# Optimization experiments

Measured on AMD Instinct MI355X. Metric: run time of the kernel, lower is better.

The kernel has to match this reference:

```python
import jax, jax.numpy as jnp
import numpy as np


def setup_inputs() -> dict:
    key = jax.random.key(0)
    k0, k1, k2, k3 = jax.random.split(key, 4)
    B, L, H, E, D = 8, 1024, 8, 64, 64
    queries = jax.random.normal(k0, (B, L, H, E), dtype=jnp.float32)
    keys = jax.random.normal(k1, (B, L, H, E), dtype=jnp.float32)
    values = jax.random.normal(k2, (B, L, H, D), dtype=jnp.float32)
    # sigma is a divisor inside exp(-dist/sigma); keep it strictly positive
    sigma = jax.random.uniform(k3, (B, H, L), dtype=jnp.float32, minval=0.1, maxval=2.0)
    return {"queries": queries, "keys": keys, "values": values, "sigma": sigma}


def reference(queries, keys, values, sigma):
    B, L, H, E = queries.shape
    S = keys.shape[1]
    scale = 1.0 / float(E) ** 0.5  # self.scale is None -> 1/sqrt(E)

    # series association: masked scaled softmax(QK^T)
    scores = jnp.einsum('blhe,bshe->bhls', queries, keys)  # (B,H,L,S)
    causal = jnp.triu(jnp.ones((L, S), dtype=bool), k=1)   # TriangularCausalMask
    scores = jnp.where(causal[None, None], -jnp.inf, scores)
    series_association = jax.nn.softmax(scale * scores, axis=-1)  # dropout p=0.0

    # prior association: Gaussian-kernel over |i-j|, sigma indexed by column s
    # prior[b,i,s] = mean_h exp(-|i-s| / sigma[b,h,s]), then row-normalized
    dist = jnp.abs(jnp.arange(L)[:, None] - jnp.arange(S)[None, :]).astype(queries.dtype)  # (L,S)
    prior = jnp.exp(-dist[None, None] / sigma[:, :, None, :]).mean(axis=1)  # (B,L,S)
    prior_association = prior / prior.sum(axis=-1, keepdims=True)

    V = jnp.einsum('bhls,bshd->blhd', series_association, values)  # (B,L,H,D)
    return V, series_association, prior_association
```

## Files before the change

kernel.cpp:

```cpp
#include <hip/hip_runtime.h>
#include <hip/hip_bf16.h>

#define B_ 8
#define L_ 1024
#define H_ 8
#define E_ 64
#define CL2E 0.18033688f

typedef __attribute__((ext_vector_type(8))) short bf8v;
typedef __attribute__((ext_vector_type(4))) float f32x4;

__device__ __forceinline__ short f2bf(float x) {
    union { float f; unsigned u; } c; c.f = x;
    const unsigned r = (c.u + 0x7fffu + ((c.u >> 16) & 1u)) >> 16;
    return (short)r;
}

__global__ __launch_bounds__(256) void kconv_kernel(const float* __restrict__ K,
                                                    short* __restrict__ Kb) {
    const int g = blockIdx.x * 256 + threadIdx.x;
    const float4 v = *((const float4*)K + g);
    const int e4 = g & 15, h = (g >> 4) & 7, l = (g >> 7) & 1023, b = g >> 17;
    short4 o; o.x = f2bf(v.x); o.y = f2bf(v.y); o.z = f2bf(v.z); o.w = f2bf(v.w);
    *(short4*)(Kb + (((size_t)(b * 8 + h)) << 16) + l * 64 + (e4 << 2)) = o;
}

__global__ __launch_bounds__(256) void vtrans_kernel(const float* __restrict__ V,
                                                     short* __restrict__ VT) {
    const int bx = blockIdx.x;
    const int bh = bx >> 4; const int l0 = (bx & 15) << 6;
    const int b = bh >> 3, h = bh & 7;
    const int t = threadIdx.x;
    __shared__ float lds[64][65];
    {
        const int r = t >> 2, cq = t & 3;
        const float* src = V + ((size_t)((b * 1024 + l0 + r) * 8) + h) * 64 + (cq << 4);
#pragma unroll
        for (int j = 0; j < 4; ++j) {
            const float4 v = *(const float4*)(src + (j << 2));
            const int d = (cq << 4) + (j << 2);
            lds[r][d] = v.x; lds[r][d + 1] = v.y; lds[r][d + 2] = v.z; lds[r][d + 3] = v.w;
        }
    }
    __syncthreads();
    {
        const int d = t >> 2, lq = t & 3;
        short tmp[16];
#pragma unroll
        for (int k = 0; k < 16; ++k) tmp[k] = f2bf(lds[(lq << 4) + k][d]);
        short* dst = VT + ((size_t)bh << 16) + d * 1024 + l0 + (lq << 4);
        *(bf8v*)dst = *(bf8v*)tmp;
        *(bf8v*)(dst + 8) = *(bf8v*)(tmp + 8);
    }
}

__global__ __launch_bounds__(256) void prior_kernel(const float* __restrict__ sigma,
                                                    float* __restrict__ outP) {
    const int bx = blockIdx.x;
    const int b  = bx >> 8;
    const int i0 = (bx & 255) << 2;
    const int t  = threadIdx.x;
    const int s0 = t << 2;

    __shared__ float wred[4][4];
    __shared__ float sinv[4];

    const float* sb = sigma + (size_t)b * H_ * L_;
    float wv[8][4];
#pragma unroll
    for (int h = 0; h < 8; ++h) {
        const float4 sg = *(const float4*)(sb + h * L_ + s0);
        wv[h][0] = -1.4426950408889634f * __builtin_amdgcn_rcpf(sg.x);
        wv[h][1] = -1.4426950408889634f * __builtin_amdgcn_rcpf(sg.y);
        wv[h][2] = -1.4426950408889634f * __builtin_amdgcn_rcpf(sg.z);
        wv[h][3] = -1.4426950408889634f * __builtin_amdgcn_rcpf(sg.w);
    }
    float acc[4][4];
#pragma unroll
    for (int row = 0; row < 4; ++row)
#pragma unroll
        for (int j = 0; j < 4; ++j) acc[row][j] = 0.f;
#pragma unroll
    for (int h = 0; h < 8; ++h)
#pragma unroll
        for (int row = 0; row < 4; ++row)
#pragma unroll
            for (int j = 0; j < 4; ++j) {
                int di = (i0 + row) - (s0 + j);
                const float dist = (float)(di < 0 ? -di : di);
                acc[row][j] += __builtin_amdgcn_exp2f(dist * wv[h][j]);
            }
    float tsum[4];
#pragma unroll
    for (int row = 0; row < 4; ++row) {
        float v = acc[row][0] + acc[row][1] + acc[row][2] + acc[row][3];
#pragma unroll
        for (int off = 1; off < 64; off <<= 1) v += __shfl_xor(v, off);
        tsum[row] = v;
    }
    if ((t & 63) == 0) {
#pragma unroll
        for (int row = 0; row < 4; ++row) wred[t >> 6][row] = tsum[row];
    }
    __syncthreads();
    if (t < 4) sinv[t] = 1.f / (wred[0][t] + wred[1][t] + wred[2][t] + wred[3][t]);
    __syncthreads();
#pragma unroll
    for (int row = 0; row < 4; ++row) {
        const float iv = sinv[row];
        float4 o;
        o.x = acc[row][0] * iv; o.y = acc[row][1] * iv;
        o.z = acc[row][2] * iv; o.w = acc[row][3] * iv;
        *(float4*)(outP + (size_t)(b * L_ + i0 + row) * L_ + s0) = o;
    }
}

__global__ __launch_bounds__(256, 4) void attn_kernel(const float* __restrict__ Q,
                                                      const short* __restrict__ Kbf,
                                                      const short* __restrict__ VTbf,
                                                      float* __restrict__ outV,
                                                      float* __restrict__ outS) {
    const int bx = blockIdx.x;
    const int qt = 15 - (bx >> 6);
    const int bh = bx & 63;
    const int b = bh >> 3, h = bh & 7;
    const int q0 = qt << 6;
    const int t = threadIdx.x;
    const int lane = t & 63, w = t >> 6;
    const int l15 = lane & 15, l4 = lane >> 4;
    const int nch = qt + 1;

    __shared__ __align__(16) short Klds[4096];
    __shared__ __align__(16) short Vlds[4096];
    __shared__ __align__(16) short Plds[4096];

    const short* Kb = Kbf + ((size_t)bh << 16);
    const short* Vb = VTbf + ((size_t)bh << 16);

    const int srow = lane >> 3;
    const int sslot = lane & 7;
    const int pslot = sslot ^ srow;

    bf8v aq0, aq1;
    {
        const float* Qrow = Q + ((size_t)((b * 1024 + q0 + 16 * w + l15) * 8) + h) * 64 + l4 * 8;
#pragma unroll
        for (int j = 0; j < 8; ++j) aq0[j] = f2bf(Qrow[j]);
#pragma unroll
        for (int j = 0; j < 8; ++j) aq1[j] = f2bf(Qrow[32 + j]);
    }

    float* outSb = outS + ((size_t)bh << 20) + (size_t)q0 * 1024;

    {
        const int cend = nch << 6;
        const float4 z4 = make_float4(0.f, 0.f, 0.f, 0.f);
        for (int col = cend + (lane << 2); col < 1024; col += 256) {
            float* rp = outSb + (size_t)(16 * w) * 1024 + col;
#pragma unroll
            for (int rr = 0; rr < 16; ++rr) *(float4*)(rp + (size_t)rr * 1024) = z4;
        }
    }

    float sum4[4] = {0.f, 0.f, 0.f, 0.f};
    for (int c = 0; c < nch; ++c) {
        const int s0 = c << 6;
        __syncthreads();
#pragma unroll
        for (int p = 0; p < 2; ++p) {
            const int krow = 16 * w + 8 * p + srow;
            const bf8v kv = *(const bf8v*)(Kb + (size_t)(s0 + krow) * 64 + sslot * 8);
            *(bf8v*)((char*)Klds + krow * 128 + (pslot << 4)) = kv;
        }
        __syncthreads();
        const bool diag = (c == qt);
#pragma unroll
        for (int cb = 0; cb < 4; ++cb) {
            const int krow = (cb << 4) + l15;
            const char* kp = (char*)Klds + krow * 128;
            const int sw = (krow & 7) << 4;
            const bf8v b0 = *(const bf8v*)(kp + ((l4 << 4) ^ sw));
            const bf8v b1 = *(const bf8v*)(kp + ((64 + (l4 << 4)) ^ sw));
            f32x4 acc = {0.f, 0.f, 0.f, 0.f};
            acc = __builtin_amdgcn_mfma_f32_16x16x32_bf16(aq0, b0, acc, 0, 0, 0);
            acc = __builtin_amdgcn_mfma_f32_16x16x32_bf16(aq1, b1, acc, 0, 0, 0);
#pragma unroll
            for (int r = 0; r < 4; ++r) {
                float e = __builtin_amdgcn_exp2f(acc[r] * CL2E);
                if (diag && ((cb << 4) + l15 > 16 * w + (l4 << 2) + r)) e = 0.f;
                sum4[r] += e;
            }
        }
    }
#pragma unroll
    for (int r = 0; r < 4; ++r) {
        float v = sum4[r];
        v += __shfl_xor(v, 1); v += __shfl_xor(v, 2);
        v += __shfl_xor(v, 4); v += __shfl_xor(v, 8);
        sum4[r] = v;
    }
    float inv4[4];
#pragma unroll
    for (int r = 0; r < 4; ++r) inv4[r] = __builtin_amdgcn_rcpf(sum4[r]);

    f32x4 oacc[4];
#pragma unroll
    for (int db = 0; db < 4; ++db) oacc[db] = (f32x4){0.f, 0.f, 0.f, 0.f};

    short* Pw = Plds + (w << 10);
    float* sbase = outSb + (size_t)(16 * w + (l4 << 2)) * 1024 + l15;

    for (int c = 0; c < nch; ++c) {
        const int s0 = c << 6;
        __syncthreads();
#pragma unroll
        for (int p = 0; p < 2; ++p) {
            const int krow = 16 * w + 8 * p + srow;
            const bf8v kv = *(const bf8v*)(Kb + (size_t)(s0 + krow) * 64 + sslot * 8);
            *(bf8v*)((char*)Klds + krow * 128 + (pslot << 4)) = kv;
            const bf8v vv = *(const bf8v*)(Vb + (size_t)krow * 1024 + s0 + sslot * 8);
            *(bf8v*)((char*)Vlds + krow * 128 + (pslot << 4)) = vv;
        }
        __syncthreads();
        const bool diag = (c == qt);
#pragma unroll
        for (int cb = 0; cb < 4; ++cb) {
            const int krow = (cb << 4) + l15;
            const char* kp = (char*)Klds + krow * 128;
            const int sw = (krow & 7) << 4;
            const bf8v b0 = *(const bf8v*)(kp + ((l4 << 4) ^ sw));
            const bf8v b1 = *(const bf8v*)(kp + ((64 + (l4 << 4)) ^ sw));
            f32x4 acc = {0.f, 0.f, 0.f, 0.f};
            acc = __builtin_amdgcn_mfma_f32_16x16x32_bf16(aq0, b0, acc, 0, 0, 0);
            acc = __builtin_amdgcn_mfma_f32_16x16x32_bf16(aq1, b1, acc, 0, 0, 0);
#pragma unroll
            for (int r = 0; r < 4; ++r) {
                float e = __builtin_amdgcn_exp2f(acc[r] * CL2E);
                if (diag && ((cb << 4) + l15 > 16 * w + (l4 << 2) + r)) e = 0.f;
                const float pv = e * inv4[r];
                sbase[(size_t)r * 1024 + s0 + (cb << 4)] = pv;
                const int row = (l4 << 2) + r;
                const int byte = row * 128 +
                                 ((((cb << 1) + (l15 >> 3)) ^ (row & 7)) << 4) +
                                 ((l15 & 7) << 1);
                *(short*)((char*)Pw + byte) = f2bf(pv);
            }
        }
        const int swp = (l15 & 7) << 4;
        const bf8v p0 = *(const bf8v*)((char*)Pw + l15 * 128 + ((l4 << 4) ^ swp));
        const bf8v p1 = *(const bf8v*)((char*)Pw + l15 * 128 + (((4 + l4) << 4) ^ swp));
#pragma unroll
        for (int db = 0; db < 4; ++db) {
            const int vrow = (db << 4) + l15;
            const char* vp = (char*)Vlds + vrow * 128;
            const int swv = (vrow & 7) << 4;
            const bf8v v0 = *(const bf8v*)(vp + ((l4 << 4) ^ swv));
            const bf8v v1 = *(const bf8v*)(vp + (((4 + l4) << 4) ^ swv));
            oacc[db] = __builtin_amdgcn_mfma_f32_16x16x32_bf16(p0, v0, oacc[db], 0, 0, 0);
            oacc[db] = __builtin_amdgcn_mfma_f32_16x16x32_bf16(p1, v1, oacc[db], 0, 0, 0);
        }
    }

#pragma unroll
    for (int db = 0; db < 4; ++db)
#pragma unroll
        for (int r = 0; r < 4; ++r)
            outV[((size_t)((b * 1024 + q0 + 16 * w + (l4 << 2) + r) * 8) + h) * 64 +
                 (db << 4) + l15] = oacc[db][r];
}

extern "C" void kernel_launch(void* const* d_in, const int* in_sizes, int n_in,
                              void* d_out, int out_size, void* d_ws, size_t ws_size,
                              hipStream_t stream) {
    const float* Q     = (const float*)d_in[0];
    const float* K     = (const float*)d_in[1];
    const float* V     = (const float*)d_in[2];
    const float* sigma = (const float*)d_in[3];

    float* out  = (float*)d_out;
    float* outV = out;
    float* outS = out + (size_t)B_ * L_ * H_ * E_;
    float* outP = outS + (size_t)B_ * H_ * L_ * L_;

    short* Kbf = (short*)outP;
    short* VTb = Kbf + ((size_t)64 << 16);

    kconv_kernel<<<dim3(4096), dim3(256), 0, stream>>>(K, Kbf);
    vtrans_kernel<<<dim3(1024), dim3(256), 0, stream>>>(V, VTb);
    attn_kernel<<<dim3(1024), dim3(256), 0, stream>>>(Q, Kbf, VTb, outV, outS);
    prior_kernel<<<dim3(B_ * (L_ / 4)), dim3(256), 0, stream>>>(sigma, outP);
}
```

Baseline: 400.7 us.

## Double-buffer K/V LDS staging with register prefetch and fuse prep kernels

```diff
diff --git a/kernel.cpp b/kernel.cpp
--- a/kernel.cpp
+++ b/kernel.cpp
@@ -16,36 +16,43 @@
     return (short)r;
 }
 
-__global__ __launch_bounds__(256) void kconv_kernel(const float* __restrict__ K,
-                                                    short* __restrict__ Kb) {
-    const int g = blockIdx.x * 256 + threadIdx.x;
-    const float4 v = *((const float4*)K + g);
-    const int e4 = g & 15, h = (g >> 4) & 7, l = (g >> 7) & 1023, b = g >> 17;
-    short4 o; o.x = f2bf(v.x); o.y = f2bf(v.y); o.z = f2bf(v.z); o.w = f2bf(v.w);
-    *(short4*)(Kb + (((size_t)(b * 8 + h)) << 16) + l * 64 + (e4 << 2)) = o;
-}
-
-__global__ __launch_bounds__(256) void vtrans_kernel(const float* __restrict__ V,
-                                                     short* __restrict__ VT) {
+__global__ __launch_bounds__(256) void prep_kernel(const float* __restrict__ K,
+                                                   const float* __restrict__ V,
+                                                   short* __restrict__ Kb,
+                                                   short* __restrict__ VT) {
     const int bx = blockIdx.x;
     const int bh = bx >> 4; const int l0 = (bx & 15) << 6;
     const int b = bh >> 3, h = bh & 7;
     const int t = threadIdx.x;
     __shared__ float lds[64][65];
-    {
-        const int r = t >> 2, cq = t & 3;
-        const float* src = V + ((size_t)((b * 1024 + l0 + r) * 8) + h) * 64 + (cq << 4);
+
+    const int r = t >> 2, cq = t & 3;
+    {
+        const float* vsrc = V + ((size_t)((b * 1024 + l0 + r) * 8) + h) * 64 + (cq << 4);
 #pragma unroll
         for (int j = 0; j < 4; ++j) {
-            const float4 v = *(const float4*)(src + (j << 2));
+            const float4 v = *(const float4*)(vsrc + (j << 2));
             const int d = (cq << 4) + (j << 2);
             lds[r][d] = v.x; lds[r][d + 1] = v.y; lds[r][d + 2] = v.z; lds[r][d + 3] = v.w;
         }
     }
+    {
+        const float* ksrc = K + ((size_t)((b * 1024 + l0 + r) * 8) + h) * 64 + (cq << 4);
+        short tk[16] __attribute__((aligned(16)));
+#pragma unroll
+        for (int j = 0; j < 4; ++j) {
+            const float4 v = *(const float4*)(ksrc + (j << 2));
+            tk[(j << 2) + 0] = f2bf(v.x); tk[(j << 2) + 1] = f2bf(v.y);
+            tk[(j << 2) + 2] = f2bf(v.z); tk[(j << 2) + 3] = f2bf(v.w);
+        }
+        short* kdst = Kb + ((size_t)bh << 16) + (l0 + r) * 64 + (cq << 4);
+        *(bf8v*)kdst = *(bf8v*)tk;
+        *(bf8v*)(kdst + 8) = *(bf8v*)(tk + 8);
+    }
     __syncthreads();
     {
         const int d = t >> 2, lq = t & 3;
-        short tmp[16];
+        short tmp[16] __attribute__((aligned(16)));
 #pragma unroll
         for (int k = 0; k < 16; ++k) tmp[k] = f2bf(lds[(lq << 4) + k][d]);
         short* dst = VT + ((size_t)bh << 16) + d * 1024 + l0 + (lq << 4);
@@ -130,8 +137,7 @@
     const int l15 = lane & 15, l4 = lane >> 4;
     const int nch = qt + 1;
 
-    __shared__ __align__(16) short Klds[4096];
-    __shared__ __align__(16) short Vlds[4096];
+    __shared__ __align__(16) short stage[2][8192];
     __shared__ __align__(16) short Plds[4096];
 
     const short* Kb = Kbf + ((size_t)bh << 16);
@@ -140,6 +146,11 @@
     const int srow = lane >> 3;
     const int sslot = lane & 7;
     const int pslot = sslot ^ srow;
+    const int krow0 = 16 * w + srow;
+    const int stb0 = krow0 * 128 + (pslot << 4);
+    const int stb1 = stb0 + 8 * 128;
+    const short* kbase = Kb + krow0 * 64 + sslot * 8;
+    const short* vbase = Vb + krow0 * 1024 + sslot * 8;
 
     bf8v aq0, aq1;
     {
@@ -152,32 +163,39 @@
 
     float* outSb = outS + ((size_t)bh << 20) + (size_t)q0 * 1024;
 
+    bf8v kA, kB, vA, vB;
+
+    kA = *(const bf8v*)(kbase);
+    kB = *(const bf8v*)(kbase + 512);
     {
         const int cend = nch << 6;
-        const float4 z4 = make_float4(0.f, 0.f, 0.f, 0.f);
+        const f32x4 z4 = {0.f, 0.f, 0.f, 0.f};
         for (int col = cend + (lane << 2); col < 1024; col += 256) {
             float* rp = outSb + (size_t)(16 * w) * 1024 + col;
 #pragma unroll
-            for (int rr = 0; rr < 16; ++rr) *(float4*)(rp + (size_t)rr * 1024) = z4;
-        }
-    }
+            for (int rr = 0; rr < 16; ++rr)
+                __builtin_nontemporal_store(z4, (f32x4*)(rp + (size_t)rr * 1024));
+        }
+    }
+    {
+        char* d0 = (char*)stage[0];
+        *(bf8v*)(d0 + stb0) = kA;
+        *(bf8v*)(d0 + stb1) = kB;
+    }
+    __syncthreads();
 
     float sum4[4] = {0.f, 0.f, 0.f, 0.f};
     for (int c = 0; c < nch; ++c) {
-        const int s0 = c << 6;
-        __syncthreads();
-#pragma unroll
-        for (int p = 0; p < 2; ++p) {
-            const int krow = 16 * w + 8 * p + srow;
-            const bf8v kv = *(const bf8v*)(Kb + (size_t)(s0 + krow) * 64 + sslot * 8);
-            *(bf8v*)((char*)Klds + krow * 128 + (pslot << 4)) = kv;
-        }
-        __syncthreads();
+        if (c + 1 < nch) {
+            kA = *(const bf8v*)(kbase + (size_t)(c + 1) * 4096);
+            kB = *(const bf8v*)(kbase + (size_t)(c + 1) * 4096 + 512);
+        }
+        const char* kt = (const char*)stage[c & 1];
         const bool diag = (c == qt);
 #pragma unroll
         for (int cb = 0; cb < 4; ++cb) {
             const int krow = (cb << 4) + l15;
-            const char* kp = (char*)Klds + krow * 128;
+            const char* kp = kt + krow * 128;
             const int sw = (krow & 7) << 4;
             const bf8v b0 = *(const bf8v*)(kp + ((l4 << 4) ^ sw));
             const bf8v b1 = *(const bf8v*)(kp + ((64 + (l4 << 4)) ^ sw));
@@ -191,7 +209,16 @@
                 sum4[r] += e;
             }
         }
-    }
+        if (c + 1 < nch) {
+            char* dn = (char*)stage[(c + 1) & 1];
+            *(bf8v*)(dn + stb0) = kA;
+            *(bf8v*)(dn + stb1) = kB;
+        }
+        __syncthreads();
+    }
+
+    vA = *(const bf8v*)(vbase + (nch - 1) * 64);
+    vB = *(const bf8v*)(vbase + (nch - 1) * 64 + 8192);
 #pragma unroll
     for (int r = 0; r < 4; ++r) {
         float v = sum4[r];
@@ -202,6 +229,12 @@
     float inv4[4];
 #pragma unroll
     for (int r = 0; r < 4; ++r) inv4[r] = __builtin_amdgcn_rcpf(sum4[r]);
+    {
+        char* sv = (char*)stage[(nch - 1) & 1] + 8192;
+        *(bf8v*)(sv + stb0) = vA;
+        *(bf8v*)(sv + stb1) = vB;
+    }
+    __syncthreads();
 
     f32x4 oacc[4];
 #pragma unroll
@@ -210,23 +243,21 @@
     short* Pw = Plds + (w << 10);
     float* sbase = outSb + (size_t)(16 * w + (l4 << 2)) * 1024 + l15;
 
-    for (int c = 0; c < nch; ++c) {
+    for (int c = nch - 1; c >= 0; --c) {
+        if (c > 0) {
+            kA = *(const bf8v*)(kbase + (size_t)(c - 1) * 4096);
+            kB = *(const bf8v*)(kbase + (size_t)(c - 1) * 4096 + 512);
+            vA = *(const bf8v*)(vbase + (c - 1) * 64);
+            vB = *(const bf8v*)(vbase + (c - 1) * 64 + 8192);
+        }
         const int s0 = c << 6;
-        __syncthreads();
-#pragma unroll
-        for (int p = 0; p < 2; ++p) {
-            const int krow = 16 * w + 8 * p + srow;
-            const bf8v kv = *(const bf8v*)(Kb + (size_t)(s0 + krow) * 64 + sslot * 8);
-            *(bf8v*)((char*)Klds + krow * 128 + (pslot << 4)) = kv;
-            const bf8v vv = *(const bf8v*)(Vb + (size_t)krow * 1024 + s0 + sslot * 8);
-            *(bf8v*)((char*)Vlds + krow * 128 + (pslot << 4)) = vv;
-        }
-        __syncthreads();
+        const char* kt = (const char*)stage[c & 1];
+        const char* vt = kt + 8192;
         const bool diag = (c == qt);
 #pragma unroll
         for (int cb = 0; cb < 4; ++cb) {
             const int krow = (cb << 4) + l15;
-            const char* kp = (char*)Klds + krow * 128;
+            const char* kp = kt + krow * 128;
             const int sw = (krow & 7) << 4;
             const bf8v b0 = *(const bf8v*)(kp + ((l4 << 4) ^ sw));
             const bf8v b1 = *(const bf8v*)(kp + ((64 + (l4 << 4)) ^ sw));
@@ -238,7 +269,7 @@
                 float e = __builtin_amdgcn_exp2f(acc[r] * CL2E);
                 if (diag && ((cb << 4) + l15 > 16 * w + (l4 << 2) + r)) e = 0.f;
                 const float pv = e * inv4[r];
-                sbase[(size_t)r * 1024 + s0 + (cb << 4)] = pv;
+                __builtin_nontemporal_store(pv, sbase + (size_t)r * 1024 + s0 + (cb << 4));
                 const int row = (l4 << 2) + r;
                 const int byte = row * 128 +
                                  ((((cb << 1) + (l15 >> 3)) ^ (row & 7)) << 4) +
@@ -252,13 +283,21 @@
 #pragma unroll
         for (int db = 0; db < 4; ++db) {
             const int vrow = (db << 4) + l15;
-            const char* vp = (char*)Vlds + vrow * 128;
+            const char* vp = vt + vrow * 128;
             const int swv = (vrow & 7) << 4;
             const bf8v v0 = *(const bf8v*)(vp + ((l4 << 4) ^ swv));
             const bf8v v1 = *(const bf8v*)(vp + (((4 + l4) << 4) ^ swv));
             oacc[db] = __builtin_amdgcn_mfma_f32_16x16x32_bf16(p0, v0, oacc[db], 0, 0, 0);
             oacc[db] = __builtin_amdgcn_mfma_f32_16x16x32_bf16(p1, v1, oacc[db], 0, 0, 0);
         }
+        if (c > 0) {
+            char* dn = (char*)stage[(c - 1) & 1];
+            *(bf8v*)(dn + stb0) = kA;
+            *(bf8v*)(dn + stb1) = kB;
+            *(bf8v*)(dn + 8192 + stb0) = vA;
+            *(bf8v*)(dn + 8192 + stb1) = vB;
+        }
+        __syncthreads();
     }
 
 #pragma unroll
@@ -285,8 +324,7 @@
     short* Kbf = (short*)outP;
     short* VTb = Kbf + ((size_t)64 << 16);
 
-    kconv_kernel<<<dim3(4096), dim3(256), 0, stream>>>(K, Kbf);
-    vtrans_kernel<<<dim3(1024), dim3(256), 0, stream>>>(V, VTb);
+    prep_kernel<<<dim3(1024), dim3(256), 0, stream>>>(K, V, Kbf, VTb);
     attn_kernel<<<dim3(1024), dim3(256), 0, stream>>>(Q, Kbf, VTb, outV, outS);
     prior_kernel<<<dim3(B_ * (L_ / 4)), dim3(256), 0, stream>>>(sigma, outP);
 }
```

Result: no change. 405.7 us (+1.2%).
